# Kernel optimization log

Hardware: AMD Instinct MI355X
Metric: run time of the kernel (lower is better)

Reference implementation:

```python
import jax, jax.numpy as jnp
import numpy as np

B, F, P, DM = 1, 16, 256, 1024            # batch, frames, patches, mm_hidden_size
HID = 4096                                 # config.hidden_size
DI, DSTATE, DTRANK, DCONV = 2 * DM, 16, DM // 16, 4


def _layernorm(x, w, b):
    mu = x.mean(-1, keepdims=True)
    var = ((x - mu) ** 2).mean(-1, keepdims=True)
    return (x - mu) * jax.lax.rsqrt(var + 1e-5) * w + b


def _selective_scan(u, dt, A, Bm, Cm, Dv):
    # u, dt: [b,L,d]; Bm, Cm: [b,L,n]; A: [d,n]; Dv: [d]
    def step(h, inp):
        dt_t, B_t, C_t, u_t = inp  # [b,d],[b,n],[b,n],[b,d]
        h = jnp.exp(dt_t[..., None] * A) * h + (dt_t * u_t)[..., None] * B_t[:, None, :]
        return h, jnp.einsum('bdn,bn->bd', h, C_t)
    h0 = jnp.zeros((u.shape[0], A.shape[0], A.shape[1]), u.dtype)
    _, ys = jax.lax.scan(step, h0, (jnp.swapaxes(dt, 0, 1), jnp.swapaxes(Bm, 0, 1),
                                    jnp.swapaxes(Cm, 0, 1), jnp.swapaxes(u, 0, 1)))
    return jnp.swapaxes(ys, 0, 1) + u * Dv


def _mamba_block(x, ln_w, ln_b, in_proj_w, conv_w, conv_b, x_proj_w,
                 dt_proj_w, dt_proj_b, A_log, D_param, out_proj_w):
    res = x
    x = _layernorm(x, ln_w, ln_b)
    xz = x @ in_proj_w                       # [b,L,2*DI]
    xin, z = jnp.split(xz, 2, axis=-1)
    xt = jnp.swapaxes(xin, 1, 2)             # [b,DI,L]
    xt = jax.lax.conv_general_dilated(xt, conv_w[:, None, :], (1,), [(DCONV - 1, 0)],
                                      dimension_numbers=('NCH', 'OIH', 'NCH'),
                                      feature_group_count=DI)
    xt = xt + conv_b[:, None]
    u = jax.nn.silu(jnp.swapaxes(xt, 1, 2))  # [b,L,DI]
    x_dbl = u @ x_proj_w                     # [b,L,DTRANK+2*DSTATE]
    dt_raw, Bm, Cm = jnp.split(x_dbl, [DTRANK, DTRANK + DSTATE], axis=-1)
    dt = jax.nn.softplus(dt_raw @ dt_proj_w + dt_proj_b)
    A = -jnp.exp(A_log)
    y = _selective_scan(u, dt, A, Bm, Cm, D_param)
    y = y * jax.nn.silu(z)
    return res + y @ out_proj_w


def setup_inputs() -> dict:
    key = jax.random.key(0)
    ks = jax.random.split(key, 8)
    s = 0.02
    return {
        'vst': jax.random.normal(ks[0], (B, F, P, DM), jnp.float32),
        'ln_w': jnp.ones((DM,), jnp.float32), 'ln_b': jnp.zeros((DM,), jnp.float32),
        'in_proj_w': jax.random.normal(ks[1], (DM, 2 * DI), jnp.float32) * s,
        'conv_w': jax.random.normal(ks[2], (DI, DCONV), jnp.float32) * s,
        'conv_b': jnp.zeros((DI,), jnp.float32),
        'x_proj_w': jax.random.normal(ks[3], (DI, DTRANK + 2 * DSTATE), jnp.float32) * s,
        'dt_proj_w': jax.random.normal(ks[4], (DTRANK, DI), jnp.float32) * s,
        'dt_proj_b': jnp.full((DI,), -4.6, jnp.float32),  # softplus ~ 0.01
        'A_log': jnp.log(jnp.tile(jnp.arange(1, DSTATE + 1, dtype=jnp.float32), (DI, 1))),
        'D_param': jnp.ones((DI,), jnp.float32),
        'out_proj_w': jax.random.normal(ks[5], (DI, DM), jnp.float32) * s,
        'fln_w': jnp.ones((DM,), jnp.float32), 'fln_b': jnp.zeros((DM,), jnp.float32),
        'mlp_w1': jax.random.normal(ks[6], (DM, HID), jnp.float32) * s,
        'mlp_b1': jnp.zeros((HID,), jnp.float32),
        'mlp_w2': jax.random.normal(ks[7], (HID, HID), jnp.float32) * s,
        'mlp_b2': jnp.zeros((HID,), jnp.float32),
    }


def reference(vst, ln_w, ln_b, in_proj_w, conv_w, conv_b, x_proj_w, dt_proj_w,
              dt_proj_b, A_log, D_param, out_proj_w, fln_w, fln_b,
              mlp_w1, mlp_b1, mlp_w2, mlp_b2):
    b, f, p, d = vst.shape
    h = w = int(p ** 0.5)
    # the chain of rearranges in the source is a net reshape to b (f h w) d
    x = vst.reshape(b, f * h * w, d)
    x = _mamba_block(x, ln_w, ln_b, in_proj_w, conv_w, conv_b, x_proj_w,
                     dt_proj_w, dt_proj_b, A_log, D_param, out_proj_w)
    x = _layernorm(x, fln_w, fln_b)
    # AvgPool3d kernel=(1,4,4), stride=(1,4,4) over (f,h,w)
    x = x.reshape(b, f, h // 4, 4, w // 4, 4, d).mean(axis=(3, 5))
    x = x.reshape(b, f * (h // 4) * (w // 4), d)
    y = jax.nn.gelu(x @ mlp_w1 + mlp_b1, approximate=False)
    return y @ mlp_w2 + mlp_b2
```

## Files before the change

### kernel.cpp

```cpp
#include <hip/hip_runtime.h>
#include <hip/hip_bf16.h>
#include <math.h>

typedef __hip_bfloat16 bf16_t;
typedef __attribute__((ext_vector_type(8))) short short8;
typedef __attribute__((ext_vector_type(4))) float f32x4;

#define L_SEQ   4096
#define DMODEL  1024
#define DI      2048
#define NST     16
#define DTRANK  64
#define XDBL_N  96
#define HID     4096
#define CHUNK   32
#define NCHUNK  128
#define POOLED_ROWS 256

__device__ __forceinline__ void async_load16(const bf16_t* g, bf16_t* l) {
    __builtin_amdgcn_global_load_lds(
        (const __attribute__((address_space(1))) void*)g,
        (__attribute__((address_space(3))) void*)l,
        16, 0, 0);
}

__global__ __launch_bounds__(256)
void transpose_all_kernel(const float* __restrict__ j0, bf16_t* __restrict__ o0,
                          const float* __restrict__ j1, bf16_t* __restrict__ o1,
                          const float* __restrict__ j2, bf16_t* __restrict__ o2,
                          const float* __restrict__ j3, bf16_t* __restrict__ o3,
                          const float* __restrict__ j4, bf16_t* __restrict__ o4,
                          const float* __restrict__ j5, bf16_t* __restrict__ o5) {
    int b = blockIdx.x;
    const float* in; bf16_t* out; int K, N, Npad, local;
    if (b < 4096)        { in = j0; out = o0; K = 1024; N = 4096; Npad = 4096; local = b; }
    else if (b < 4352)   { in = j1; out = o1; K = 2048; N = 96;   Npad = 128;  local = b - 4096; }
    else if (b < 4480)   { in = j2; out = o2; K = 64;   N = 2048; Npad = 2048; local = b - 4352; }
    else if (b < 6528)   { in = j3; out = o3; K = 2048; N = 1024; Npad = 1024; local = b - 4480; }
    else if (b < 10624)  { in = j4; out = o4; K = 1024; N = 4096; Npad = 4096; local = b - 6528; }
    else                 { in = j5; out = o5; K = 4096; N = 4096; Npad = 4096; local = b - 10624; }
    int nb = Npad / 32;
    int k0 = (local / nb) * 32, n0 = (local % nb) * 32;

    __shared__ float t[32][33];
    int tx = threadIdx.x & 31, ty = threadIdx.x >> 5;
#pragma unroll
    for (int i = 0; i < 4; i++) {
        int k = k0 + ty + i * 8, n = n0 + tx;
        t[ty + i * 8][tx] = (n < N) ? in[(size_t)k * N + n] : 0.f;
    }
    __syncthreads();
#pragma unroll
    for (int i = 0; i < 4; i++) {
        int n = n0 + ty + i * 8, k = k0 + tx;
        if (n < Npad) out[(size_t)n * K + k] = __float2bfloat16(t[tx][ty + i * 8]);
    }
}

__global__ __launch_bounds__(256)
void ln_kernel(const float* __restrict__ x, const float* __restrict__ w,
               const float* __restrict__ b, bf16_t* __restrict__ out) {
    int row = blockIdx.x;
    int tid = threadIdx.x;
    const float* xr = x + (size_t)row * DMODEL;
    float v[4];
    float s = 0.f, ss = 0.f;
#pragma unroll
    for (int e = 0; e < 4; e++) {
        v[e] = xr[tid + e * 256];
        s += v[e];
        ss += v[e] * v[e];
    }
#pragma unroll
    for (int off = 32; off > 0; off >>= 1) {
        s  += __shfl_down(s, off);
        ss += __shfl_down(ss, off);
    }
    __shared__ float rs[4], rss[4];
    int wid = tid >> 6;
    if ((tid & 63) == 0) { rs[wid] = s; rss[wid] = ss; }
    __syncthreads();
    s  = rs[0] + rs[1] + rs[2] + rs[3];
    ss = rss[0] + rss[1] + rss[2] + rss[3];
    float mu  = s * (1.f / DMODEL);
    float var = ss * (1.f / DMODEL) - mu * mu;
    float inv = rsqrtf(var + 1e-5f);
#pragma unroll
    for (int e = 0; e < 4; e++) {
        int col = tid + e * 256;
        out[(size_t)row * DMODEL + col] =
            __float2bfloat16((v[e] - mu) * inv * w[col] + b[col]);
    }
}

__global__ __launch_bounds__(256)
void ln_pool_kernel(const float* __restrict__ x, const float* __restrict__ w,
                    const float* __restrict__ b, bf16_t* __restrict__ pooled) {
    int p = blockIdx.x;
    int tid = threadIdx.x;
    int f = p >> 4, i4 = (p >> 2) & 3, j4 = p & 3;
    __shared__ float rs[4], rss[4];
    float acc[4] = {0.f, 0.f, 0.f, 0.f};
    float wv[4], bv[4];
#pragma unroll
    for (int e = 0; e < 4; e++) { wv[e] = w[tid + e * 256]; bv[e] = b[tid + e * 256]; }
    for (int r16 = 0; r16 < 16; r16++) {
        int ii = r16 >> 2, jj = r16 & 3;
        int row = f * 256 + (i4 * 4 + ii) * 16 + j4 * 4 + jj;
        const float* xr = x + (size_t)row * DMODEL;
        float v[4];
        float s = 0.f, ss = 0.f;
#pragma unroll
        for (int e = 0; e < 4; e++) {
            v[e] = xr[tid + e * 256];
            s += v[e];
            ss += v[e] * v[e];
        }
#pragma unroll
        for (int off = 32; off > 0; off >>= 1) {
            s  += __shfl_down(s, off);
            ss += __shfl_down(ss, off);
        }
        int wid = tid >> 6;
        if ((tid & 63) == 0) { rs[wid] = s; rss[wid] = ss; }
        __syncthreads();
        s  = rs[0] + rs[1] + rs[2] + rs[3];
        ss = rss[0] + rss[1] + rss[2] + rss[3];
        float mu  = s * (1.f / DMODEL);
        float var = ss * (1.f / DMODEL) - mu * mu;
        float inv = rsqrtf(var + 1e-5f);
#pragma unroll
        for (int e = 0; e < 4; e++)
            acc[e] += (v[e] - mu) * inv * wv[e] + bv[e];
        __syncthreads();
    }
#pragma unroll
    for (int e = 0; e < 4; e++)
        pooled[(size_t)p * DMODEL + tid + e * 256] = __float2bfloat16(acc[e] * (1.f / 16.f));
}

template <int EPI>
__global__ __launch_bounds__(256, 2)
void mfma_gemm(const bf16_t* __restrict__ A, int lda,
               const bf16_t* __restrict__ Bt, int ldb,
               int K,
               float* __restrict__ Cf, bf16_t* __restrict__ Cb, int ldc,
               const float* __restrict__ bias, const float* __restrict__ res) {
    __shared__ bf16_t Asl[128 * 32];
    __shared__ bf16_t Bsl[128 * 32];
    const int tid = threadIdx.x;
    const int l = tid & 63, w = tid >> 6;
    const int m0 = blockIdx.y * 128, n0 = blockIdx.x * 128;
    const int wm = (w >> 1) * 64, wn = (w & 1) * 64;

    const int srow = tid >> 2;
    const int skc = (tid & 3) * 8;
    const bf16_t* Ag = A + (size_t)(m0 + srow) * lda + skc;
    const bf16_t* Bg = Bt + (size_t)(n0 + srow) * ldb + skc;
    bf16_t* As0 = Asl + (size_t)(w * 64) * 8;
    bf16_t* As1 = Asl + (size_t)(256 + w * 64) * 8;
    bf16_t* Bs0 = Bsl + (size_t)(w * 64) * 8;
    bf16_t* Bs1 = Bsl + (size_t)(256 + w * 64) * 8;

    f32x4 acc[4][4];
#pragma unroll
    for (int i = 0; i < 4; i++)
#pragma unroll
        for (int j = 0; j < 4; j++) acc[i][j] = (f32x4){0.f, 0.f, 0.f, 0.f};

    const short8* Asv = (const short8*)Asl;
    const short8* Bsv = (const short8*)Bsl;
    const int fr = l >> 4;
    const int fc = l & 15;

    for (int k0 = 0; k0 < K; k0 += 32) {
        __syncthreads();
        async_load16(Ag, As0);
        async_load16(Ag + (size_t)64 * lda, As1);
        async_load16(Bg, Bs0);
        async_load16(Bg + (size_t)64 * ldb, Bs1);
        Ag += 32; Bg += 32;
        __syncthreads();

        short8 a[4], b[4];
#pragma unroll
        for (int im = 0; im < 4; im++)
            a[im] = Asv[(wm + im * 16 + fc) * 4 + fr];
#pragma unroll
        for (int in = 0; in < 4; in++)
            b[in] = Bsv[(wn + in * 16 + fc) * 4 + fr];
#pragma unroll
        for (int im = 0; im < 4; im++)
#pragma unroll
            for (int in = 0; in < 4; in++)
                acc[im][in] = __builtin_amdgcn_mfma_f32_16x16x32_bf16(
                    a[im], b[in], acc[im][in], 0, 0, 0);
    }

#pragma unroll
    for (int im = 0; im < 4; im++) {
        int mbase = m0 + wm + im * 16 + fr * 4;
#pragma unroll
        for (int in = 0; in < 4; in++) {
            int n = n0 + wn + in * 16 + fc;
            float bv = (EPI == 1) ? bias[n] : 0.f;
#pragma unroll
            for (int v = 0; v < 4; v++) {
                float x = acc[im][in][v];
                size_t off = (size_t)(mbase + v) * ldc + n;
                if (EPI == 0) {
                    Cb[off] = __float2bfloat16(x);
                } else if (EPI == 1) {
                    x += bv;
                    x = (x > 20.f) ? x : log1pf(__expf(x));
                    Cb[off] = __float2bfloat16(x);
                }
            }
        }
    }
}

__global__ __launch_bounds__(256, 2)
void mfma_gemm64_res(const bf16_t* __restrict__ A, int lda,
                     const bf16_t* __restrict__ Bt, int ldb,
                     int K, float* __restrict__ Cf, int ldc,
                     const float* __restrict__ res) {
    __shared__ bf16_t Asl[64 * 32];
    __shared__ bf16_t Bsl[128 * 32];
    const int tid = threadIdx.x;
    const int l = tid & 63, w = tid >> 6;
    const int m0 = blockIdx.y * 64, n0 = blockIdx.x * 128;
    const int wn = w * 32;

    const int srow = tid >> 2;
    const int skc = (tid & 3) * 8;
    const bf16_t* Ag = A + (size_t)(m0 + srow) * lda + skc;
    const bf16_t* Bg = Bt + (size_t)(n0 + srow) * ldb + skc;
    bf16_t* As0 = Asl + (size_t)(w * 64) * 8;
    bf16_t* Bs0 = Bsl + (size_t)(w * 64) * 8;
    bf16_t* Bs1 = Bsl + (size_t)(256 + w * 64) * 8;

    f32x4 acc[4][2];
#pragma unroll
    for (int i = 0; i < 4; i++)
#pragma unroll
        for (int j = 0; j < 2; j++) acc[i][j] = (f32x4){0.f, 0.f, 0.f, 0.f};

    const short8* Asv = (const short8*)Asl;
    const short8* Bsv = (const short8*)Bsl;
    const int fr = l >> 4;
    const int fc = l & 15;

    for (int k0 = 0; k0 < K; k0 += 32) {
        __syncthreads();
        async_load16(Ag, As0);
        async_load16(Bg, Bs0);
        async_load16(Bg + (size_t)64 * ldb, Bs1);
        Ag += 32; Bg += 32;
        __syncthreads();

        short8 a[4], b[2];
#pragma unroll
        for (int im = 0; im < 4; im++)
            a[im] = Asv[(im * 16 + fc) * 4 + fr];
#pragma unroll
        for (int in = 0; in < 2; in++)
            b[in] = Bsv[(wn + in * 16 + fc) * 4 + fr];
#pragma unroll
        for (int im = 0; im < 4; im++)
#pragma unroll
            for (int in = 0; in < 2; in++)
                acc[im][in] = __builtin_amdgcn_mfma_f32_16x16x32_bf16(
                    a[im], b[in], acc[im][in], 0, 0, 0);
    }

#pragma unroll
    for (int im = 0; im < 4; im++) {
        int mbase = m0 + im * 16 + fr * 4;
#pragma unroll
        for (int in = 0; in < 2; in++) {
            int n = n0 + wn + in * 16 + fc;
#pragma unroll
            for (int v = 0; v < 4; v++) {
                size_t off = (size_t)(mbase + v) * ldc + n;
                Cf[off] = acc[im][in][v] + res[off];
            }
        }
    }
}

__global__ __launch_bounds__(256, 2)
void mfma_gemm_splitk(const bf16_t* __restrict__ A, int lda,
                      const bf16_t* __restrict__ Bt, int ldb,
                      int Kper, float* __restrict__ Cpart, int ldc,
                      size_t pstride) {
    __shared__ bf16_t Asl[128 * 32];
    __shared__ bf16_t Bsl[128 * 32];
    const int tid = threadIdx.x;
    const int l = tid & 63, w = tid >> 6;
    const int m0 = blockIdx.y * 128, n0 = blockIdx.x * 128;
    const int wm = (w >> 1) * 64, wn = (w & 1) * 64;
    const int kbase = blockIdx.z * Kper;

    const int srow = tid >> 2;
    const int skc = (tid & 3) * 8;
    const bf16_t* Ag = A + (size_t)(m0 + srow) * lda + kbase + skc;
    const bf16_t* Bg = Bt + (size_t)(n0 + srow) * ldb + kbase + skc;
    bf16_t* As0 = Asl + (size_t)(w * 64) * 8;
    bf16_t* As1 = Asl + (size_t)(256 + w * 64) * 8;
    bf16_t* Bs0 = Bsl + (size_t)(w * 64) * 8;
    bf16_t* Bs1 = Bsl + (size_t)(256 + w * 64) * 8;

    f32x4 acc[4][4];
#pragma unroll
    for (int i = 0; i < 4; i++)
#pragma unroll
        for (int j = 0; j < 4; j++) acc[i][j] = (f32x4){0.f, 0.f, 0.f, 0.f};

    const short8* Asv = (const short8*)Asl;
    const short8* Bsv = (const short8*)Bsl;
    const int fr = l >> 4;
    const int fc = l & 15;

    for (int k0 = 0; k0 < Kper; k0 += 32) {
        __syncthreads();
        async_load16(Ag, As0);
        async_load16(Ag + (size_t)64 * lda, As1);
        async_load16(Bg, Bs0);
        async_load16(Bg + (size_t)64 * ldb, Bs1);
        Ag += 32; Bg += 32;
        __syncthreads();

        short8 a[4], b[4];
#pragma unroll
        for (int im = 0; im < 4; im++)
            a[im] = Asv[(wm + im * 16 + fc) * 4 + fr];
#pragma unroll
        for (int in = 0; in < 4; in++)
            b[in] = Bsv[(wn + in * 16 + fc) * 4 + fr];
#pragma unroll
        for (int im = 0; im < 4; im++)
#pragma unroll
            for (int in = 0; in < 4; in++)
                acc[im][in] = __builtin_amdgcn_mfma_f32_16x16x32_bf16(
                    a[im], b[in], acc[im][in], 0, 0, 0);
    }

    float* Cz = Cpart + (size_t)blockIdx.z * pstride;
#pragma unroll
    for (int im = 0; im < 4; im++) {
        int mbase = m0 + wm + im * 16 + fr * 4;
#pragma unroll
        for (int in = 0; in < 4; in++) {
            int n = n0 + wn + in * 16 + fc;
#pragma unroll
            for (int v = 0; v < 4; v++)
                Cz[(size_t)(mbase + v) * ldc + n] = acc[im][in][v];
        }
    }
}

template <int S, int EPI>
__global__ __launch_bounds__(256)
void reduce_splitk(const float* __restrict__ part, size_t pstride, int ldp,
                   int M, int N, float* __restrict__ outf, bf16_t* __restrict__ outb,
                   int ldo, const float* __restrict__ bias) {
    int idx = blockIdx.x * 256 + threadIdx.x;
    if (idx >= M * N) return;
    int r = idx / N, c = idx - r * N;
    float s = 0.f;
#pragma unroll
    for (int z = 0; z < S; z++)
        s += part[(size_t)z * pstride + (size_t)r * ldp + c];
    size_t o = (size_t)r * ldo + c;
    if (EPI == 0) {
        outf[o] = s;
        outb[o] = __float2bfloat16(s);
    } else if (EPI == 1) {
        s += bias[c];
        s = 0.5f * s * (1.f + erff(s * 0.70710678118654752f));
        outb[o] = __float2bfloat16(s);
    } else {
        outf[o] = s + bias[c];
    }
}

__global__ __launch_bounds__(256)
void conv_silu_kernel(const bf16_t* __restrict__ xz, const float* __restrict__ cw,
                      const float* __restrict__ cb, bf16_t* __restrict__ u) {
    int idx = blockIdx.x * 256 + threadIdx.x;
    if (idx >= L_SEQ * DI) return;
    int ch = idx & (DI - 1);
    int l  = idx >> 11;
    float acc = cb[ch];
#pragma unroll
    for (int k = 0; k < 4; k++) {
        int ls = l - 3 + k;
        if (ls >= 0)
            acc += cw[ch * 4 + k] * __bfloat162float(xz[(size_t)ls * (2 * DI) + ch]);
    }
    u[idx] = __float2bfloat16(acc / (1.f + __expf(-acc)));
}

__global__ __launch_bounds__(64)
void scan_pass1(const bf16_t* __restrict__ dt, const bf16_t* __restrict__ u,
                const float* __restrict__ x_dbl, const float* __restrict__ A_log,
                float* __restrict__ Pw, float* __restrict__ Sw) {
    int c = blockIdx.x;
    int d = blockIdx.y * 64 + threadIdx.x;
    int l0 = c * CHUNK;
    __shared__ float sB[CHUNK * NST];
    for (int i = threadIdx.x; i < CHUNK * NST; i += 64) {
        int l = i >> 4, n = i & 15;
        sB[i] = x_dbl[(size_t)(l0 + l) * XDBL_N + DTRANK + n];
    }
    __syncthreads();
    float Areg[NST], h[NST];
#pragma unroll
    for (int n = 0; n < NST; n++) {
        Areg[n] = -__expf(A_log[d * NST + n]);
        h[n] = 0.f;
    }
    float dts = 0.f;
    float dtl = __bfloat162float(dt[(size_t)l0 * DI + d]);
    float ul  = __bfloat162float(u[(size_t)l0 * DI + d]);
    for (int l = 0; l < CHUNK; l++) {
        float dtn = 0.f, un = 0.f;
        if (l + 1 < CHUNK) {
            int gl = l0 + l + 1;
            dtn = __bfloat162float(dt[(size_t)gl * DI + d]);
            un  = __bfloat162float(u[(size_t)gl * DI + d]);
        }
        float du = dtl * ul;
        dts += dtl;
#pragma unroll
        for (int n = 0; n < NST; n++) {
            float a = __expf(dtl * Areg[n]);
            h[n] = a * h[n] + du * sB[l * NST + n];
        }
        dtl = dtn; ul = un;
    }
    size_t base = (size_t)c * (DI * NST) + (size_t)d * NST;
#pragma unroll
    for (int n = 0; n < NST; n++) {
        Pw[base + n] = __expf(dts * Areg[n]);
        Sw[base + n] = h[n];
    }
}

__global__ __launch_bounds__(256)
void scan_pass2(const float* __restrict__ Pw, float* __restrict__ SwInit) {
    int tid = blockIdx.x * 256 + threadIdx.x;
    if (tid >= DI * NST) return;
    float h = 0.f;
    for (int c = 0; c < NCHUNK; c++) {
        size_t idx = (size_t)c * (DI * NST) + tid;
        float s = SwInit[idx];
        SwInit[idx] = h;
        h = Pw[idx] * h + s;
    }
}

__global__ __launch_bounds__(64)
void scan_pass3(const bf16_t* __restrict__ dt, const bf16_t* __restrict__ u,
                const float* __restrict__ x_dbl, const float* __restrict__ A_log,
                const float* __restrict__ Dp, const float* __restrict__ initw,
                const bf16_t* __restrict__ xz, bf16_t* __restrict__ yy) {
    int c = blockIdx.x;
    int d = blockIdx.y * 64 + threadIdx.x;
    int l0 = c * CHUNK;
    __shared__ float sBC[CHUNK * 2 * NST];
    for (int i = threadIdx.x; i < CHUNK * 2 * NST; i += 64) {
        int l = i >> 5, n = i & 31;
        sBC[i] = x_dbl[(size_t)(l0 + l) * XDBL_N + DTRANK + n];
    }
    __syncthreads();
    float Areg[NST], h[NST];
    size_t base = (size_t)c * (DI * NST) + (size_t)d * NST;
#pragma unroll
    for (int n = 0; n < NST; n++) {
        Areg[n] = -__expf(A_log[d * NST + n]);
        h[n] = initw[base + n];
    }
    float Dd = Dp[d];
    float dtl = __bfloat162float(dt[(size_t)l0 * DI + d]);
    float ul  = __bfloat162float(u[(size_t)l0 * DI + d]);
    float zv  = __bfloat162float(xz[(size_t)l0 * (2 * DI) + DI + d]);
    for (int l = 0; l < CHUNK; l++) {
        float dtn = 0.f, un = 0.f, zn = 0.f;
        if (l + 1 < CHUNK) {
            int gl = l0 + l + 1;
            dtn = __bfloat162float(dt[(size_t)gl * DI + d]);
            un  = __bfloat162float(u[(size_t)gl * DI + d]);
            zn  = __bfloat162float(xz[(size_t)gl * (2 * DI) + DI + d]);
        }
        float du = dtl * ul;
        float y = 0.f;
#pragma unroll
        for (int n = 0; n < NST; n++) {
            float a = __expf(dtl * Areg[n]);
            h[n] = a * h[n] + du * sBC[l * 32 + n];
            y += h[n] * sBC[l * 32 + NST + n];
        }
        float sz = zv / (1.f + __expf(-zv));
        yy[(size_t)(l0 + l) * DI + d] = __float2bfloat16((y + ul * Dd) * sz);
        dtl = dtn; ul = un; zv = zn;
    }
}

extern "C" void kernel_launch(void* const* d_in, const int* in_sizes, int n_in,
                              void* d_out, int out_size, void* d_ws, size_t ws_size,
                              hipStream_t stream) {
    const float* vst        = (const float*)d_in[0];
    const float* ln_w       = (const float*)d_in[1];
    const float* ln_b       = (const float*)d_in[2];
    const float* in_proj_w  = (const float*)d_in[3];
    const float* conv_w     = (const float*)d_in[4];
    const float* conv_b     = (const float*)d_in[5];
    const float* x_proj_w   = (const float*)d_in[6];
    const float* dt_proj_w  = (const float*)d_in[7];
    const float* dt_proj_b  = (const float*)d_in[8];
    const float* A_log      = (const float*)d_in[9];
    const float* D_param    = (const float*)d_in[10];
    const float* out_proj_w = (const float*)d_in[11];
    const float* fln_w      = (const float*)d_in[12];
    const float* fln_b      = (const float*)d_in[13];
    const float* mlp_w1     = (const float*)d_in[14];
    const float* mlp_b1     = (const float*)d_in[15];
    const float* mlp_w2     = (const float*)d_in[16];
    const float* mlp_b2     = (const float*)d_in[17];
    float* out = (float*)d_out;

    char* wsb = (char*)d_ws;
    size_t off = 0;
    auto alloc_bf = [&](size_t n) { bf16_t* p = (bf16_t*)(wsb + off); off += n * 2; return p; };
    auto alloc_f  = [&](size_t n) { float*  p = (float*)(wsb + off); off += n * 4; return p; };

    bf16_t* w1t  = alloc_bf((size_t)(2 * DI) * DMODEL);
    bf16_t* xpt  = alloc_bf((size_t)128 * DI);
    bf16_t* dtpt = alloc_bf((size_t)DI * DTRANK);
    bf16_t* opt  = alloc_bf((size_t)DMODEL * DI);
    bf16_t* m1t  = alloc_bf((size_t)HID * DMODEL);
    bf16_t* m2t  = alloc_bf((size_t)HID * HID);
    bf16_t* xz_bf   = alloc_bf((size_t)L_SEQ * 2 * DI);
    bf16_t* u_bf    = alloc_bf((size_t)L_SEQ * DI);
    bf16_t* dt_bf   = alloc_bf((size_t)L_SEQ * DI);
    bf16_t* xdbl_bf = alloc_bf((size_t)L_SEQ * XDBL_N);
    bf16_t* yy_bf   = alloc_bf((size_t)L_SEQ * DI);
    float*  xdbl_f  = alloc_f((size_t)L_SEQ * XDBL_N);
    float*  Pw      = alloc_f((size_t)NCHUNK * DI * NST);
    float*  Sw      = alloc_f((size_t)NCHUNK * DI * NST);
    bf16_t* xn_bf   = yy_bf;
    float*  g2part  = Pw;
    float*  x2_f    = Pw;
    bf16_t* pooled  = dt_bf;
    bf16_t* h1_bf   = dt_bf + (size_t)POOLED_ROWS * DMODEL;
    float*  g5part  = (float*)yy_bf;
    float*  g6part  = (float*)xz_bf;

    dim3 blk256(256);

    transpose_all_kernel<<<27008, blk256, 0, stream>>>(
        in_proj_w, w1t, x_proj_w, xpt, dt_proj_w, dtpt,
        out_proj_w, opt, mlp_w1, m1t, mlp_w2, m2t);

    ln_kernel<<<L_SEQ, blk256, 0, stream>>>(vst, ln_w, ln_b, xn_bf);

    mfma_gemm<0><<<dim3((2 * DI) / 128, L_SEQ / 128), blk256, 0, stream>>>(
        xn_bf, DMODEL, w1t, DMODEL, DMODEL, nullptr, xz_bf, 2 * DI, nullptr, nullptr);

    conv_silu_kernel<<<(L_SEQ * DI) / 256, blk256, 0, stream>>>(xz_bf, conv_w, conv_b, u_bf);

    mfma_gemm_splitk<<<dim3(1, L_SEQ / 128, 8), blk256, 0, stream>>>(
        u_bf, DI, xpt, DI, DI / 8, g2part, 128, (size_t)L_SEQ * 128);
    reduce_splitk<8, 0><<<(L_SEQ * XDBL_N) / 256, blk256, 0, stream>>>(
        g2part, (size_t)L_SEQ * 128, 128, L_SEQ, XDBL_N, xdbl_f, xdbl_bf, XDBL_N, nullptr);

    mfma_gemm<1><<<dim3(DI / 128, L_SEQ / 128), blk256, 0, stream>>>(
        xdbl_bf, XDBL_N, dtpt, DTRANK, DTRANK, nullptr, dt_bf, DI, dt_proj_b, nullptr);

    scan_pass1<<<dim3(NCHUNK, DI / 64), dim3(64), 0, stream>>>(
        dt_bf, u_bf, xdbl_f, A_log, Pw, Sw);
    scan_pass2<<<(DI * NST) / 256, blk256, 0, stream>>>(Pw, Sw);
    scan_pass3<<<dim3(NCHUNK, DI / 64), dim3(64), 0, stream>>>(
        dt_bf, u_bf, xdbl_f, A_log, D_param, Sw, xz_bf, yy_bf);

    mfma_gemm64_res<<<dim3(DMODEL / 128, L_SEQ / 64), blk256, 0, stream>>>(
        yy_bf, DI, opt, DI, DI, x2_f, DMODEL, vst);

    ln_pool_kernel<<<POOLED_ROWS, blk256, 0, stream>>>(x2_f, fln_w, fln_b, pooled);

    mfma_gemm_splitk<<<dim3(HID / 128, POOLED_ROWS / 128, 4), blk256, 0, stream>>>(
        pooled, DMODEL, m1t, DMODEL, DMODEL / 4, g5part, HID, (size_t)POOLED_ROWS * HID);
    reduce_splitk<4, 1><<<(POOLED_ROWS * HID) / 256, blk256, 0, stream>>>(
        g5part, (size_t)POOLED_ROWS * HID, HID, POOLED_ROWS, HID, nullptr, h1_bf, HID, mlp_b1);

    mfma_gemm_splitk<<<dim3(HID / 128, POOLED_ROWS / 128, 8), blk256, 0, stream>>>(
        h1_bf, HID, m2t, HID, HID / 8, g6part, HID, (size_t)POOLED_ROWS * HID);
    reduce_splitk<8, 2><<<(POOLED_ROWS * HID) / 256, blk256, 0, stream>>>(
        g6part, (size_t)POOLED_ROWS * HID, HID, POOLED_ROWS, HID, out, nullptr, HID, mlp_b2);
}
```

Before: 496.8 us.

## Widen weight transpose tiles, split scan state across lanes, split-K out_proj

The weight transpose kernel now uses 64x64 tiles with float4 loads and 16-byte bf16 stores, which cuts the block count and makes global accesses wider. Both scan passes now split the 16 SSM states across two half-waves, giving 128 channels per 256-thread block and more parallelism, with a shuffle to combine the y partials. The out_proj GEMM moves from a 64-row tile kernel to the 128x128 split-K kernel with two bf16 partials, and a new vectorised kernel adds the partials and the residual. Storing the partials in bf16 adds rounding error and an extra pass over memory.

```diff
diff --git a/kernel.cpp b/kernel.cpp
--- a/kernel.cpp
+++ b/kernel.cpp
@@ -24,6 +24,10 @@
         16, 0, 0);
 }
 
+__device__ __forceinline__ float bfbits2f(unsigned short b) {
+    bf16_t h; *(unsigned short*)&h = b; return __bfloat162float(h);
+}
+
 __global__ __launch_bounds__(256)
 void transpose_all_kernel(const float* __restrict__ j0, bf16_t* __restrict__ o0,
                           const float* __restrict__ j1, bf16_t* __restrict__ o1,
@@ -33,27 +37,49 @@
                           const float* __restrict__ j5, bf16_t* __restrict__ o5) {
     int b = blockIdx.x;
     const float* in; bf16_t* out; int K, N, Npad, local;
-    if (b < 4096)        { in = j0; out = o0; K = 1024; N = 4096; Npad = 4096; local = b; }
-    else if (b < 4352)   { in = j1; out = o1; K = 2048; N = 96;   Npad = 128;  local = b - 4096; }
-    else if (b < 4480)   { in = j2; out = o2; K = 64;   N = 2048; Npad = 2048; local = b - 4352; }
-    else if (b < 6528)   { in = j3; out = o3; K = 2048; N = 1024; Npad = 1024; local = b - 4480; }
-    else if (b < 10624)  { in = j4; out = o4; K = 1024; N = 4096; Npad = 4096; local = b - 6528; }
-    else                 { in = j5; out = o5; K = 4096; N = 4096; Npad = 4096; local = b - 10624; }
-    int nb = Npad / 32;
-    int k0 = (local / nb) * 32, n0 = (local % nb) * 32;
-
-    __shared__ float t[32][33];
-    int tx = threadIdx.x & 31, ty = threadIdx.x >> 5;
-#pragma unroll
-    for (int i = 0; i < 4; i++) {
-        int k = k0 + ty + i * 8, n = n0 + tx;
-        t[ty + i * 8][tx] = (n < N) ? in[(size_t)k * N + n] : 0.f;
+    if (b < 1024)       { in = j0; out = o0; K = 1024; N = 4096; Npad = 4096; local = b; }
+    else if (b < 1088)  { in = j1; out = o1; K = 2048; N = 96;   Npad = 128;  local = b - 1024; }
+    else if (b < 1120)  { in = j2; out = o2; K = 64;   N = 2048; Npad = 2048; local = b - 1088; }
+    else if (b < 1632)  { in = j3; out = o3; K = 2048; N = 1024; Npad = 1024; local = b - 1120; }
+    else if (b < 2656)  { in = j4; out = o4; K = 1024; N = 4096; Npad = 4096; local = b - 1632; }
+    else                { in = j5; out = o5; K = 4096; N = 4096; Npad = 4096; local = b - 2656; }
+    int nt = Npad >> 6;
+    int k0 = (local / nt) << 6, n0 = (local % nt) << 6;
+
+    __shared__ float t[64 * 65];
+    int tid = threadIdx.x;
+#pragma unroll
+    for (int it = 0; it < 4; it++) {
+        int slot = it * 256 + tid;
+        int kk = slot >> 4, nq = (slot & 15) * 4;
+        int gn = n0 + nq;
+        const float* src = in + (size_t)(k0 + kk) * N + gn;
+        float4 v;
+        if (gn + 3 < N) v = *(const float4*)src;
+        else {
+            v.x = (gn + 0 < N) ? src[0] : 0.f;
+            v.y = (gn + 1 < N) ? src[1] : 0.f;
+            v.z = (gn + 2 < N) ? src[2] : 0.f;
+            v.w = (gn + 3 < N) ? src[3] : 0.f;
+        }
+        t[(nq + 0) * 65 + kk] = v.x;
+        t[(nq + 1) * 65 + kk] = v.y;
+        t[(nq + 2) * 65 + kk] = v.z;
+        t[(nq + 3) * 65 + kk] = v.w;
     }
     __syncthreads();
 #pragma unroll
-    for (int i = 0; i < 4; i++) {
-        int n = n0 + ty + i * 8, k = k0 + tx;
-        if (n < Npad) out[(size_t)n * K + k] = __float2bfloat16(t[tx][ty + i * 8]);
+    for (int it = 0; it < 2; it++) {
+        int slot = it * 256 + tid;
+        int nn = slot >> 3, kc = (slot & 7) * 8;
+        const float* r = &t[nn * 65 + kc];
+        short8 o;
+#pragma unroll
+        for (int j = 0; j < 8; j++) {
+            bf16_t h = __float2bfloat16(r[j]);
+            o[j] = *(short*)&h;
+        }
+        *(short8*)(out + (size_t)(n0 + nn) * K + k0 + kc) = o;
     }
 }
 
@@ -220,79 +246,11 @@
     }
 }
 
-__global__ __launch_bounds__(256, 2)
-void mfma_gemm64_res(const bf16_t* __restrict__ A, int lda,
-                     const bf16_t* __restrict__ Bt, int ldb,
-                     int K, float* __restrict__ Cf, int ldc,
-                     const float* __restrict__ res) {
-    __shared__ bf16_t Asl[64 * 32];
-    __shared__ bf16_t Bsl[128 * 32];
-    const int tid = threadIdx.x;
-    const int l = tid & 63, w = tid >> 6;
-    const int m0 = blockIdx.y * 64, n0 = blockIdx.x * 128;
-    const int wn = w * 32;
-
-    const int srow = tid >> 2;
-    const int skc = (tid & 3) * 8;
-    const bf16_t* Ag = A + (size_t)(m0 + srow) * lda + skc;
-    const bf16_t* Bg = Bt + (size_t)(n0 + srow) * ldb + skc;
-    bf16_t* As0 = Asl + (size_t)(w * 64) * 8;
-    bf16_t* Bs0 = Bsl + (size_t)(w * 64) * 8;
-    bf16_t* Bs1 = Bsl + (size_t)(256 + w * 64) * 8;
-
-    f32x4 acc[4][2];
-#pragma unroll
-    for (int i = 0; i < 4; i++)
-#pragma unroll
-        for (int j = 0; j < 2; j++) acc[i][j] = (f32x4){0.f, 0.f, 0.f, 0.f};
-
-    const short8* Asv = (const short8*)Asl;
-    const short8* Bsv = (const short8*)Bsl;
-    const int fr = l >> 4;
-    const int fc = l & 15;
-
-    for (int k0 = 0; k0 < K; k0 += 32) {
-        __syncthreads();
-        async_load16(Ag, As0);
-        async_load16(Bg, Bs0);
-        async_load16(Bg + (size_t)64 * ldb, Bs1);
-        Ag += 32; Bg += 32;
-        __syncthreads();
-
-        short8 a[4], b[2];
-#pragma unroll
-        for (int im = 0; im < 4; im++)
-            a[im] = Asv[(im * 16 + fc) * 4 + fr];
-#pragma unroll
-        for (int in = 0; in < 2; in++)
-            b[in] = Bsv[(wn + in * 16 + fc) * 4 + fr];
-#pragma unroll
-        for (int im = 0; im < 4; im++)
-#pragma unroll
-            for (int in = 0; in < 2; in++)
-                acc[im][in] = __builtin_amdgcn_mfma_f32_16x16x32_bf16(
-                    a[im], b[in], acc[im][in], 0, 0, 0);
-    }
-
-#pragma unroll
-    for (int im = 0; im < 4; im++) {
-        int mbase = m0 + im * 16 + fr * 4;
-#pragma unroll
-        for (int in = 0; in < 2; in++) {
-            int n = n0 + wn + in * 16 + fc;
-#pragma unroll
-            for (int v = 0; v < 4; v++) {
-                size_t off = (size_t)(mbase + v) * ldc + n;
-                Cf[off] = acc[im][in][v] + res[off];
-            }
-        }
-    }
-}
-
+template <bool PBF16>
 __global__ __launch_bounds__(256, 2)
 void mfma_gemm_splitk(const bf16_t* __restrict__ A, int lda,
                       const bf16_t* __restrict__ Bt, int ldb,
-                      int Kper, float* __restrict__ Cpart, int ldc,
+                      int Kper, void* __restrict__ Cpart, int ldc,
                       size_t pstride) {
     __shared__ bf16_t Asl[128 * 32];
     __shared__ bf16_t Bsl[128 * 32];
@@ -346,7 +304,6 @@
                     a[im], b[in], acc[im][in], 0, 0, 0);
     }
 
-    float* Cz = Cpart + (size_t)blockIdx.z * pstride;
 #pragma unroll
     for (int im = 0; im < 4; im++) {
         int mbase = m0 + wm + im * 16 + fr * 4;
@@ -354,8 +311,14 @@
         for (int in = 0; in < 4; in++) {
             int n = n0 + wn + in * 16 + fc;
 #pragma unroll
-            for (int v = 0; v < 4; v++)
-                Cz[(size_t)(mbase + v) * ldc + n] = acc[im][in][v];
+            for (int v = 0; v < 4; v++) {
+                size_t o = (size_t)(mbase + v) * ldc + n;
+                if (PBF16)
+                    ((bf16_t*)Cpart)[(size_t)blockIdx.z * pstride + o] =
+                        __float2bfloat16(acc[im][in][v]);
+                else
+                    ((float*)Cpart)[(size_t)blockIdx.z * pstride + o] = acc[im][in][v];
+            }
         }
     }
 }
@@ -386,6 +349,24 @@
 }
 
 __global__ __launch_bounds__(256)
+void reduce2_res_kernel(const bf16_t* __restrict__ part, size_t pstride,
+                        const float* __restrict__ res, float* __restrict__ outf,
+                        int total4) {
+    int idx = blockIdx.x * 256 + threadIdx.x;
+    if (idx >= total4) return;
+    size_t o = (size_t)idx * 4;
+    ushort4 p0 = *(const ushort4*)((const unsigned short*)part + o);
+    ushort4 p1 = *(const ushort4*)((const unsigned short*)part + pstride + o);
+    float4 r = *(const float4*)(res + o);
+    float4 ov;
+    ov.x = bfbits2f(p0.x) + bfbits2f(p1.x) + r.x;
+    ov.y = bfbits2f(p0.y) + bfbits2f(p1.y) + r.y;
+    ov.z = bfbits2f(p0.z) + bfbits2f(p1.z) + r.z;
+    ov.w = bfbits2f(p0.w) + bfbits2f(p1.w) + r.w;
+    *(float4*)(outf + o) = ov;
+}
+
+__global__ __launch_bounds__(256)
 void conv_silu_kernel(const bf16_t* __restrict__ xz, const float* __restrict__ cw,
                       const float* __restrict__ cb, bf16_t* __restrict__ u) {
     int idx = blockIdx.x * 256 + threadIdx.x;
@@ -402,24 +383,26 @@
     u[idx] = __float2bfloat16(acc / (1.f + __expf(-acc)));
 }
 
-__global__ __launch_bounds__(64)
+__global__ __launch_bounds__(256)
 void scan_pass1(const bf16_t* __restrict__ dt, const bf16_t* __restrict__ u,
                 const float* __restrict__ x_dbl, const float* __restrict__ A_log,
                 float* __restrict__ Pw, float* __restrict__ Sw) {
     int c = blockIdx.x;
-    int d = blockIdx.y * 64 + threadIdx.x;
+    int tid = threadIdx.x;
+    int lane = tid & 63, w = tid >> 6;
+    int dloc = w * 32 + (lane & 31);
+    int n0 = (lane >> 5) * 8;
+    int d = blockIdx.y * 128 + dloc;
     int l0 = c * CHUNK;
     __shared__ float sB[CHUNK * NST];
-    for (int i = threadIdx.x; i < CHUNK * NST; i += 64) {
-        int l = i >> 4, n = i & 15;
-        sB[i] = x_dbl[(size_t)(l0 + l) * XDBL_N + DTRANK + n];
-    }
+    for (int i = tid; i < CHUNK * NST; i += 256)
+        sB[i] = x_dbl[(size_t)(l0 + (i >> 4)) * XDBL_N + DTRANK + (i & 15)];
     __syncthreads();
-    float Areg[NST], h[NST];
-#pragma unroll
-    for (int n = 0; n < NST; n++) {
-        Areg[n] = -__expf(A_log[d * NST + n]);
-        h[n] = 0.f;
+    float Areg[8], h[8];
+#pragma unroll
+    for (int j = 0; j < 8; j++) {
+        Areg[j] = -__expf(A_log[d * NST + n0 + j]);
+        h[j] = 0.f;
     }
     float dts = 0.f;
     float dtl = __bfloat162float(dt[(size_t)l0 * DI + d]);
@@ -434,17 +417,17 @@
         float du = dtl * ul;
         dts += dtl;
 #pragma unroll
-        for (int n = 0; n < NST; n++) {
-            float a = __expf(dtl * Areg[n]);
-            h[n] = a * h[n] + du * sB[l * NST + n];
+        for (int j = 0; j < 8; j++) {
+            float a = __expf(dtl * Areg[j]);
+            h[j] = a * h[j] + du * sB[l * NST + n0 + j];
         }
         dtl = dtn; ul = un;
     }
-    size_t base = (size_t)c * (DI * NST) + (size_t)d * NST;
-#pragma unroll
-    for (int n = 0; n < NST; n++) {
-        Pw[base + n] = __expf(dts * Areg[n]);
-        Sw[base + n] = h[n];
+    size_t base = ((size_t)c * DI + d) * NST + n0;
+#pragma unroll
+    for (int j = 0; j < 8; j++) {
+        Pw[base + j] = __expf(dts * Areg[j]);
+        Sw[base + j] = h[j];
     }
 }
 
@@ -461,26 +444,28 @@
     }
 }
 
-__global__ __launch_bounds__(64)
+__global__ __launch_bounds__(256)
 void scan_pass3(const bf16_t* __restrict__ dt, const bf16_t* __restrict__ u,
                 const float* __restrict__ x_dbl, const float* __restrict__ A_log,
                 const float* __restrict__ Dp, const float* __restrict__ initw,
                 const bf16_t* __restrict__ xz, bf16_t* __restrict__ yy) {
     int c = blockIdx.x;
-    int d = blockIdx.y * 64 + threadIdx.x;
+    int tid = threadIdx.x;
+    int lane = tid & 63, w = tid >> 6;
+    int dloc = w * 32 + (lane & 31);
+    int n0 = (lane >> 5) * 8;
+    int d = blockIdx.y * 128 + dloc;
     int l0 = c * CHUNK;
     __shared__ float sBC[CHUNK * 2 * NST];
-    for (int i = threadIdx.x; i < CHUNK * 2 * NST; i += 64) {
-        int l = i >> 5, n = i & 31;
-        sBC[i] = x_dbl[(size_t)(l0 + l) * XDBL_N + DTRANK + n];
-    }
+    for (int i = tid; i < CHUNK * 2 * NST; i += 256)
+        sBC[i] = x_dbl[(size_t)(l0 + (i >> 5)) * XDBL_N + DTRANK + (i & 31)];
     __syncthreads();
-    float Areg[NST], h[NST];
-    size_t base = (size_t)c * (DI * NST) + (size_t)d * NST;
-#pragma unroll
-    for (int n = 0; n < NST; n++) {
-        Areg[n] = -__expf(A_log[d * NST + n]);
-        h[n] = initw[base + n];
+    float Areg[8], h[8];
+    size_t base = ((size_t)c * DI + d) * NST + n0;
+#pragma unroll
+    for (int j = 0; j < 8; j++) {
+        Areg[j] = -__expf(A_log[d * NST + n0 + j]);
+        h[j] = initw[base + j];
     }
     float Dd = Dp[d];
     float dtl = __bfloat162float(dt[(size_t)l0 * DI + d]);
@@ -497,13 +482,15 @@
         float du = dtl * ul;
         float y = 0.f;
 #pragma unroll
-        for (int n = 0; n < NST; n++) {
-            float a = __expf(dtl * Areg[n]);
-            h[n] = a * h[n] + du * sBC[l * 32 + n];
-            y += h[n] * sBC[l * 32 + NST + n];
-        }
+        for (int j = 0; j < 8; j++) {
+            float a = __expf(dtl * Areg[j]);
+            h[j] = a * h[j] + du * sBC[l * 32 + n0 + j];
+            y += h[j] * sBC[l * 32 + NST + n0 + j];
+        }
+        y += __shfl_xor(y, 32);
         float sz = zv / (1.f + __expf(-zv));
-        yy[(size_t)(l0 + l) * DI + d] = __float2bfloat16((y + ul * Dd) * sz);
+        if ((lane >> 5) == 0)
+            yy[(size_t)(l0 + l) * DI + d] = __float2bfloat16((y + ul * Dd) * sz);
         dtl = dtn; ul = un; zv = zn;
     }
 }
@@ -553,6 +540,7 @@
     bf16_t* xn_bf   = yy_bf;
     float*  g2part  = Pw;
     float*  x2_f    = Pw;
+    bf16_t* g4part  = xz_bf;
     bf16_t* pooled  = dt_bf;
     bf16_t* h1_bf   = dt_bf + (size_t)POOLED_ROWS * DMODEL;
     float*  g5part  = (float*)yy_bf;
@@ -560,7 +548,7 @@
 
     dim3 blk256(256);
 
-    transpose_all_kernel<<<27008, blk256, 0, stream>>>(
+    transpose_all_kernel<<<6752, blk256, 0, stream>>>(
         in_proj_w, w1t, x_proj_w, xpt, dt_proj_w, dtpt,
         out_proj_w, opt, mlp_w1, m1t, mlp_w2, m2t);
 
@@ -571,7 +559,7 @@
 
     conv_silu_kernel<<<(L_SEQ * DI) / 256, blk256, 0, stream>>>(xz_bf, conv_w, conv_b, u_bf);
 
-    mfma_gemm_splitk<<<dim3(1, L_SEQ / 128, 8), blk256, 0, stream>>>(
+    mfma_gemm_splitk<false><<<dim3(1, L_SEQ / 128, 8), blk256, 0, stream>>>(
         u_bf, DI, xpt, DI, DI / 8, g2part, 128, (size_t)L_SEQ * 128);
     reduce_splitk<8, 0><<<(L_SEQ * XDBL_N) / 256, blk256, 0, stream>>>(
         g2part, (size_t)L_SEQ * 128, 128, L_SEQ, XDBL_N, xdbl_f, xdbl_bf, XDBL_N, nullptr);
@@ -579,23 +567,25 @@
     mfma_gemm<1><<<dim3(DI / 128, L_SEQ / 128), blk256, 0, stream>>>(
         xdbl_bf, XDBL_N, dtpt, DTRANK, DTRANK, nullptr, dt_bf, DI, dt_proj_b, nullptr);
 
-    scan_pass1<<<dim3(NCHUNK, DI / 64), dim3(64), 0, stream>>>(
+    scan_pass1<<<dim3(NCHUNK, DI / 128), blk256, 0, stream>>>(
         dt_bf, u_bf, xdbl_f, A_log, Pw, Sw);
     scan_pass2<<<(DI * NST) / 256, blk256, 0, stream>>>(Pw, Sw);
-    scan_pass3<<<dim3(NCHUNK, DI / 64), dim3(64), 0, stream>>>(
+    scan_pass3<<<dim3(NCHUNK, DI / 128), blk256, 0, stream>>>(
         dt_bf, u_bf, xdbl_f, A_log, D_param, Sw, xz_bf, yy_bf);
 
-    mfma_gemm64_res<<<dim3(DMODEL / 128, L_SEQ / 64), blk256, 0, stream>>>(
-        yy_bf, DI, opt, DI, DI, x2_f, DMODEL, vst);
+    mfma_gemm_splitk<true><<<dim3(DMODEL / 128, L_SEQ / 128, 2), blk256, 0, stream>>>(
+        yy_bf, DI, opt, DI, DI / 2, g4part, DMODEL, (size_t)L_SEQ * DMODEL);
+    reduce2_res_kernel<<<(L_SEQ * DMODEL / 4) / 256, blk256, 0, stream>>>(
+        g4part, (size_t)L_SEQ * DMODEL, vst, x2_f, L_SEQ * DMODEL / 4);
 
     ln_pool_kernel<<<POOLED_ROWS, blk256, 0, stream>>>(x2_f, fln_w, fln_b, pooled);
 
-    mfma_gemm_splitk<<<dim3(HID / 128, POOLED_ROWS / 128, 4), blk256, 0, stream>>>(
+    mfma_gemm_splitk<false><<<dim3(HID / 128, POOLED_ROWS / 128, 4), blk256, 0, stream>>>(
         pooled, DMODEL, m1t, DMODEL, DMODEL / 4, g5part, HID, (size_t)POOLED_ROWS * HID);
     reduce_splitk<4, 1><<<(POOLED_ROWS * HID) / 256, blk256, 0, stream>>>(
         g5part, (size_t)POOLED_ROWS * HID, HID, POOLED_ROWS, HID, nullptr, h1_bf, HID, mlp_b1);
 
-    mfma_gemm_splitk<<<dim3(HID / 128, POOLED_ROWS / 128, 8), blk256, 0, stream>>>(
+    mfma_gemm_splitk<false><<<dim3(HID / 128, POOLED_ROWS / 128, 8), blk256, 0, stream>>>(
         h1_bf, HID, m2t, HID, HID / 8, g6part, HID, (size_t)POOLED_ROWS * HID);
     reduce_splitk<8, 2><<<(POOLED_ROWS * HID) / 256, blk256, 0, stream>>>(
         g6part, (size_t)POOLED_ROWS * HID, HID, POOLED_ROWS, HID, out, nullptr, HID, mlp_b2);
```

After: 493.1 us. Within noise of the previous version (-0.7%).
